# Kernel tuning notes

Measured on AMD Instinct MI355X. Metric: run time of the kernel, lower is better.

Reference implementation:

```python
import jax, jax.numpy as jnp
import numpy as np

BINS = 10
LOSS_WEIGHT = 1.0
B = 8388608  # batch size
C = 2        # class num (hardcoded in the torch module's one-hot scatter)


def setup_inputs() -> dict:
    key = jax.random.key(0)
    k1, k2, k3 = jax.random.split(key, 3)
    pred = jax.random.normal(k1, (B, C), dtype=jnp.float32)
    target = jax.random.randint(k2, (B,), 0, 2, dtype=jnp.int64)
    # label_weight: 1 if valid, 0 if ignored (random 0/1 mask as float)
    label_weight = jax.random.randint(k3, (B, C), 0, 2).astype(jnp.float32)
    return {"pred": pred, "target": target, "label_weight": label_weight}


def reference(pred, target, label_weight):
    # one-hot target: torch scatter_(1, target, 1) over 2 classes
    t = jax.nn.one_hot(target, C, dtype=jnp.float32)  # [B, 2]
    # gradient norm g = |softmax(pred).detach() - target_onehot|
    g = jnp.abs(jax.lax.stop_gradient(jax.nn.softmax(pred, axis=1)) - t)  # [B, 2]
    valid = label_weight > 0
    valid_f = valid.astype(jnp.float32)
    total = jnp.maximum(valid_f.sum(), 1.0)
    # bin index: edges are i/bins with last edge nudged by 1e-6; uniform bins so
    # floor(g*bins) clipped to bins-1 reproduces the loop's (>= low) & (<= high)
    # assignment (ties on interior edges resolve to the upper bin, matching the
    # later-iteration overwrite in the torch loop).
    bin_ids = jnp.minimum((g * BINS).astype(jnp.int32), BINS - 1)  # [B, 2]
    # per-bin valid counts (histogram)
    counts = jnp.zeros((BINS,), jnp.float32).at[bin_ids].add(valid_f)
    n = jnp.maximum((counts > 0).sum().astype(jnp.float32), 1.0)
    # GHM weights: total / num_in_bin / n for valid entries, 0 otherwise
    w = jnp.where(valid, total / jnp.maximum(counts[bin_ids], 1.0) / n, 0.0)
    w = jax.lax.stop_gradient(w)
    # weighted BCE-with-logits, reduction='sum'
    bce = jnp.maximum(pred, 0.0) - pred * t + jnp.log1p(jnp.exp(-jnp.abs(pred)))
    loss = (w * bce).sum() / total
    return loss * LOSS_WEIGHT
```

## Files before the change

kernel.cpp:

```cpp
#include <hip/hip_runtime.h>

#define BINS 10
#define TPB  256
#define NCOPY 8


__device__ __forceinline__ void ghm_row(float p0, float p1, int t, float w0, float w1,
                                        unsigned long long* hrow)
{
    float z = (t == 0) ? (p1 - p0) : (p0 - p1);
    float e = __expf(-z);
    float g = __fdividef(1.0f, 1.0f + e);
    int bin = min((int)(g * 10.0f), BINS - 1);

    float l0 = __logf(1.0f + __expf(-fabsf(p0)));
    float l1 = __logf(1.0f + __expf(-fabsf(p1)));
    float bce0 = fmaxf(p0, 0.0f) - ((t == 0) ? p0 : 0.0f) + l0;
    float bce1 = fmaxf(p1, 0.0f) - ((t == 1) ? p1 : 0.0f) + l1;

    bool v0 = (w0 > 0.0f);
    bool v1 = (w1 > 0.0f);
    float wsum = (v0 ? bce0 : 0.0f) + (v1 ? bce1 : 0.0f);
    unsigned long long cnt = (unsigned long long)((int)v0 + (int)v1);
    unsigned long long packed = (cnt << 48)
        | (unsigned long long)(unsigned int)(wsum * 1048576.0f + 0.5f);
    if (packed) atomicAdd(&hrow[bin], packed);
}

__global__ __launch_bounds__(TPB) void ghm_stage1(
    const float* __restrict__ pred, const int* __restrict__ target,
    const float* __restrict__ lw, unsigned long long* __restrict__ partial, int B)
{
    __shared__ unsigned long long h[NCOPY][BINS];
    if (threadIdx.x < NCOPY * BINS)
        ((unsigned long long*)h)[threadIdx.x] = 0ULL;
    __syncthreads();

    unsigned long long* hrow = h[threadIdx.x >> 5];

    const float4* p4 = (const float4*)pred;
    const float4* w4 = (const float4*)lw;
    const int2*   t2 = (const int2*)target;

    const int npairs = B >> 1;
    const int stride = gridDim.x * blockDim.x;
    for (int i = blockIdx.x * blockDim.x + threadIdx.x; i < npairs; i += stride) {
        float4 p = p4[i];
        float4 w = w4[i];
        int2   t = t2[i];
        ghm_row(p.x, p.y, t.x, w.x, w.y, hrow);
        ghm_row(p.z, p.w, t.y, w.z, w.w, hrow);
    }
    if ((B & 1) && blockIdx.x == 0 && threadIdx.x == 0) {
        int r = B - 1;
        ghm_row(pred[2 * r], pred[2 * r + 1], target[r], lw[2 * r], lw[2 * r + 1], h[0]);
    }
    __syncthreads();

    if (threadIdx.x < BINS) {
        unsigned long long v = 0;
#pragma unroll
        for (int c = 0; c < NCOPY; ++c) v += h[c][threadIdx.x];
        partial[blockIdx.x * BINS + threadIdx.x] = v;
    }
}

__global__ __launch_bounds__(TPB) void ghm_stage2(
    const unsigned long long* __restrict__ partial, float* __restrict__ out, int nb)
{
    double dsum[BINS];
    double dcnt[BINS];
#pragma unroll
    for (int b = 0; b < BINS; ++b) { dsum[b] = 0.0; dcnt[b] = 0.0; }

    for (int i = threadIdx.x; i < nb; i += TPB) {
#pragma unroll
        for (int b = 0; b < BINS; ++b) {
            unsigned long long p = partial[i * BINS + b];
            dcnt[b] += (double)(p >> 48);
            dsum[b] += (double)(p & ((1ULL << 48) - 1)) * (1.0 / 1048576.0);
        }
    }

#pragma unroll
    for (int b = 0; b < BINS; ++b) {
        for (int off = 32; off > 0; off >>= 1) {
            dsum[b] += __shfl_down(dsum[b], off);
            dcnt[b] += __shfl_down(dcnt[b], off);
        }
    }

    __shared__ double ss[4][BINS];
    __shared__ double sc[4][BINS];
    const int wid  = threadIdx.x >> 6;
    const int lane = threadIdx.x & 63;
    if (lane == 0) {
#pragma unroll
        for (int b = 0; b < BINS; ++b) { ss[wid][b] = dsum[b]; sc[wid][b] = dcnt[b]; }
    }
    __syncthreads();

    if (threadIdx.x == 0) {
        double loss = 0.0;
        int n = 0;
        for (int b = 0; b < BINS; ++b) {
            double S = ss[0][b] + ss[1][b] + ss[2][b] + ss[3][b];
            double C = sc[0][b] + sc[1][b] + sc[2][b] + sc[3][b];
            if (C > 0.0) { ++n; loss += S / C; }
        }
        if (n == 0) n = 1;
        out[0] = (float)(loss / (double)n);
    }
}

extern "C" void kernel_launch(void* const* d_in, const int* in_sizes, int n_in,
                              void* d_out, int out_size, void* d_ws, size_t ws_size,
                              hipStream_t stream)
{
    const float* pred   = (const float*)d_in[0];
    const int*   target = (const int*)d_in[1];
    const float* lw     = (const float*)d_in[2];
    const int B = in_sizes[1];

    int nb = 2048;
    size_t need = (size_t)nb * BINS * sizeof(unsigned long long);
    if (ws_size < need) nb = (int)(ws_size / (BINS * sizeof(unsigned long long)));

    unsigned long long* partial = (unsigned long long*)d_ws;

    ghm_stage1<<<nb, TPB, 0, stream>>>(pred, target, lw, partial, B);
    ghm_stage2<<<1, TPB, 0, stream>>>(partial, (float*)d_out, nb);
}
```

Before: 40.53 us.

## Replace shared-memory atomic histogram with per-thread register bins and wave reductions

Each thread now accumulates per-bin loss sums and counts in 20 float registers via predicated adds, instead of issuing 64-bit packed atomics to shared-memory histogram copies. Blocks reduce these with wavefront shuffles and a small shared-memory pass, then write float2 partials that stage 2 sums in double. This removes the LDS atomic contention and the fixed-point packing, at the cost of 20 extra conditional adds per row, more register pressure, and float rather than fixed-point per-thread accumulation.

New measurement: 44.06 us. 8.7% more time.

```diff
diff --git a/kernel.cpp b/kernel.cpp
--- a/kernel.cpp
+++ b/kernel.cpp
@@ -2,11 +2,11 @@
 
 #define BINS 10
 #define TPB  256
-#define NCOPY 8
+#define NBLK 2048
 
 
 __device__ __forceinline__ void ghm_row(float p0, float p1, int t, float w0, float w1,
-                                        unsigned long long* hrow)
+                                        float* __restrict__ s, float* __restrict__ c)
 {
     float z = (t == 0) ? (p1 - p0) : (p0 - p1);
     float e = __expf(-z);
@@ -21,22 +21,23 @@
     bool v0 = (w0 > 0.0f);
     bool v1 = (w1 > 0.0f);
     float wsum = (v0 ? bce0 : 0.0f) + (v1 ? bce1 : 0.0f);
-    unsigned long long cnt = (unsigned long long)((int)v0 + (int)v1);
-    unsigned long long packed = (cnt << 48)
-        | (unsigned long long)(unsigned int)(wsum * 1048576.0f + 0.5f);
-    if (packed) atomicAdd(&hrow[bin], packed);
+    float cntf = (float)((int)v0 + (int)v1);
+
+#pragma unroll
+    for (int b = 0; b < BINS; ++b) {
+        bool m = (bin == b);
+        s[b] += m ? wsum : 0.0f;
+        c[b] += m ? cntf : 0.0f;
+    }
 }
 
 __global__ __launch_bounds__(TPB) void ghm_stage1(
     const float* __restrict__ pred, const int* __restrict__ target,
-    const float* __restrict__ lw, unsigned long long* __restrict__ partial, int B)
+    const float* __restrict__ lw, float2* __restrict__ partial, int B)
 {
-    __shared__ unsigned long long h[NCOPY][BINS];
-    if (threadIdx.x < NCOPY * BINS)
-        ((unsigned long long*)h)[threadIdx.x] = 0ULL;
-    __syncthreads();
-
-    unsigned long long* hrow = h[threadIdx.x >> 5];
+    float s[BINS], c[BINS];
+#pragma unroll
+    for (int b = 0; b < BINS; ++b) { s[b] = 0.0f; c[b] = 0.0f; }
 
     const float4* p4 = (const float4*)pred;
     const float4* w4 = (const float4*)lw;
@@ -48,25 +49,43 @@
         float4 p = p4[i];
         float4 w = w4[i];
         int2   t = t2[i];
-        ghm_row(p.x, p.y, t.x, w.x, w.y, hrow);
-        ghm_row(p.z, p.w, t.y, w.z, w.w, hrow);
+        ghm_row(p.x, p.y, t.x, w.x, w.y, s, c);
+        ghm_row(p.z, p.w, t.y, w.z, w.w, s, c);
     }
     if ((B & 1) && blockIdx.x == 0 && threadIdx.x == 0) {
         int r = B - 1;
-        ghm_row(pred[2 * r], pred[2 * r + 1], target[r], lw[2 * r], lw[2 * r + 1], h[0]);
+        ghm_row(pred[2 * r], pred[2 * r + 1], target[r], lw[2 * r], lw[2 * r + 1], s, c);
+    }
+
+#pragma unroll
+    for (int b = 0; b < BINS; ++b) {
+#pragma unroll
+        for (int off = 32; off > 0; off >>= 1) {
+            s[b] += __shfl_down(s[b], off);
+            c[b] += __shfl_down(c[b], off);
+        }
+    }
+
+    __shared__ float ss[4][BINS];
+    __shared__ float sc[4][BINS];
+    const int wid  = threadIdx.x >> 6;
+    const int lane = threadIdx.x & 63;
+    if (lane == 0) {
+#pragma unroll
+        for (int b = 0; b < BINS; ++b) { ss[wid][b] = s[b]; sc[wid][b] = c[b]; }
     }
     __syncthreads();
 
     if (threadIdx.x < BINS) {
-        unsigned long long v = 0;
-#pragma unroll
-        for (int c = 0; c < NCOPY; ++c) v += h[c][threadIdx.x];
-        partial[blockIdx.x * BINS + threadIdx.x] = v;
+        int b = threadIdx.x;
+        float S = ss[0][b] + ss[1][b] + ss[2][b] + ss[3][b];
+        float C = sc[0][b] + sc[1][b] + sc[2][b] + sc[3][b];
+        partial[blockIdx.x * BINS + b] = make_float2(S, C);
     }
 }
 
 __global__ __launch_bounds__(TPB) void ghm_stage2(
-    const unsigned long long* __restrict__ partial, float* __restrict__ out, int nb)
+    const float2* __restrict__ partial, float* __restrict__ out, int nb)
 {
     double dsum[BINS];
     double dcnt[BINS];
@@ -76,9 +95,9 @@
     for (int i = threadIdx.x; i < nb; i += TPB) {
 #pragma unroll
         for (int b = 0; b < BINS; ++b) {
-            unsigned long long p = partial[i * BINS + b];
-            dcnt[b] += (double)(p >> 48);
-            dsum[b] += (double)(p & ((1ULL << 48) - 1)) * (1.0 / 1048576.0);
+            float2 p = partial[i * BINS + b];
+            dsum[b] += (double)p.x;
+            dcnt[b] += (double)p.y;
         }
     }
 
@@ -122,11 +141,11 @@
     const float* lw     = (const float*)d_in[2];
     const int B = in_sizes[1];
 
-    int nb = 2048;
-    size_t need = (size_t)nb * BINS * sizeof(unsigned long long);
-    if (ws_size < need) nb = (int)(ws_size / (BINS * sizeof(unsigned long long)));
+    int nb = NBLK;
+    size_t need = (size_t)nb * BINS * sizeof(float2);
+    if (ws_size < need) nb = (int)(ws_size / (BINS * sizeof(float2)));
 
-    unsigned long long* partial = (unsigned long long*)d_ws;
+    float2* partial = (float2*)d_ws;
 
     ghm_stage1<<<nb, TPB, 0, stream>>>(pred, target, lw, partial, B);
     ghm_stage2<<<1, TPB, 0, stream>>>(partial, (float*)d_out, nb);
```
